# Optimization experiments

Hardware: AMD Instinct MI355X
Metric: run time of the kernel (lower is better)

## Reference

```python
import jax, jax.numpy as jnp
import numpy as np

N_NODES = 100000
N_EDGES = 3200000
IN_DIM = 128
OUT_DIM = 128
BN_EPS = 1e-5
FILL_VALUE = 1.0  # improved_gcn=False -> self-loop weight 1.0 (2.0 if improved)


def setup_inputs() -> dict:
    key = jax.random.key(0)
    k1, k2, k3, k4 = jax.random.split(key, 4)
    node_features = jax.random.normal(k1, (N_NODES, IN_DIM), dtype=jnp.float32)
    edge_index = jax.random.randint(k2, (2, N_EDGES), 0, N_NODES, dtype=jnp.int64)
    edge_weight = jax.random.uniform(k3, (N_EDGES,), dtype=jnp.float32)
    # Glorot init like PyG GCNConv
    W = jax.random.normal(k4, (IN_DIM, OUT_DIM), dtype=jnp.float32) * np.sqrt(2.0 / (IN_DIM + OUT_DIM))
    b = jnp.zeros((OUT_DIM,), dtype=jnp.float32)
    gamma = jnp.ones((OUT_DIM,), dtype=jnp.float32)
    beta = jnp.zeros((OUT_DIM,), dtype=jnp.float32)
    return {"node_features": node_features, "edge_index": edge_index,
            "edge_weight": edge_weight, "W": W, "b": b, "gamma": gamma, "beta": beta}


def reference(node_features, edge_index, edge_weight, W, b, gamma, beta):
    N = node_features.shape[0]
    dt = node_features.dtype
    # --- gcn_norm: add self loops, symmetric normalization ---
    loop = jnp.arange(N, dtype=edge_index.dtype)
    row = jnp.concatenate([edge_index[0], loop])  # source
    col = jnp.concatenate([edge_index[1], loop])  # target (aggregation dim)
    w = jnp.concatenate([edge_weight.astype(dt), jnp.full((N,), FILL_VALUE, dtype=dt)])
    deg = jax.ops.segment_sum(w, col, num_segments=N)
    dinv = jnp.where(deg > 0, jax.lax.rsqrt(deg), 0.0).astype(dt)
    norm = dinv[row] * w * dinv[col]  # [E+N]
    # --- linear transform then message passing (scatter-add into targets) ---
    x = node_features @ W  # [N, out_dim]
    msg = x[row] * norm[:, None]  # [E+N, out_dim] gather
    out = jax.ops.segment_sum(msg, col, num_segments=N) + b
    # --- relu ---
    h = jax.nn.relu(out)
    # --- BatchNorm1d (training-mode batch statistics, biased variance) ---
    mean = jnp.mean(h, axis=0)
    var = jnp.mean(jnp.square(h - mean), axis=0)
    h = (h - mean) * jax.lax.rsqrt(var + BN_EPS) * gamma + beta
    # dropout is identity in eval / deterministic reference
    return h
```

## Files before the change

### kernel.cpp

```cpp
#include <hip/hip_runtime.h>
#include <hip/hip_bf16.h>


#define BKT_BITS 7
#define BKT_SZ 128
#define MAX_BKT 1024
#define CHUNK 8192

typedef __attribute__((ext_vector_type(8))) short bf16x8;
typedef __attribute__((ext_vector_type(4))) float f32x4;

__device__ __forceinline__ unsigned bf16rn(float f) {
    unsigned x = __float_as_uint(f);
    return (x + 0x7fffu + ((x >> 16) & 1u)) >> 16;
}
__device__ __forceinline__ float bflo(unsigned u) { return __uint_as_float(u << 16); }
__device__ __forceinline__ float bfhi(unsigned u) { return __uint_as_float(u & 0xffff0000u); }

__global__ __launch_bounds__(256) void k_bhist2(const int* __restrict__ col,
        int* __restrict__ blkoff, int E, int nb, int nbc) {
    __shared__ int h[MAX_BKT];
    for (int i = threadIdx.x; i < nb; i += 256) h[i] = 0;
    __syncthreads();
    int base = blockIdx.x * CHUNK, lim = min(base + CHUNK, E);
    for (int e = base + threadIdx.x; e < lim; e += 256)
        atomicAdd(&h[col[e] >> BKT_BITS], 1);
    __syncthreads();
    for (int i = threadIdx.x; i < nb; i += 256)
        blkoff[(size_t)i * nbc + blockIdx.x] = h[i];
}

__global__ void k_bscan2a(int* __restrict__ blkoff, int* __restrict__ btot,
                          int nb, int nbc) {
    int b = blockIdx.x * 256 + threadIdx.x;
    if (b >= nb) return;
    int* p = blkoff + (size_t)b * nbc;
    int run = 0;
#pragma unroll 4
    for (int i = 0; i < nbc; ++i) { int c = p[i]; p[i] = run; run += c; }
    btot[b] = run;
}

__global__ __launch_bounds__(1024) void k_bscan2b(const int* __restrict__ btot,
        int* __restrict__ bbase, int* __restrict__ ptr, float* __restrict__ sums,
        int nb, int N, int E) {
    __shared__ int ls[1024];
    int t = threadIdx.x;
    int v = (t < nb) ? btot[t] : 0;
    ls[t] = v;
    __syncthreads();
    for (int off = 1; off < 1024; off <<= 1) {
        int u = (t >= off) ? ls[t - off] : 0;
        __syncthreads();
        ls[t] += u;
        __syncthreads();
    }
    if (t < nb) bbase[t] = ls[t] - v;
    if (t == nb - 1) bbase[nb] = ls[t];
    if (t == 0) ptr[N] = E;
    if (t < 512) sums[t] = 0.0f;
}

__global__ __launch_bounds__(256) void k_passA3(
        const int* __restrict__ row, const int* __restrict__ col,
        const float* __restrict__ w, const int* __restrict__ blkoff,
        const int* __restrict__ bbase, unsigned* __restrict__ tmp,
        int E, int nb, int nbc) {
    __shared__ int cur[MAX_BKT];
    for (int i = threadIdx.x; i < nb; i += 256)
        cur[i] = bbase[i] + blkoff[(size_t)i * nbc + blockIdx.x];
    __syncthreads();
    int base = blockIdx.x * CHUNK, lim = min(base + CHUNK, E);
    for (int e = base + threadIdx.x; e < lim; e += 256) {
        int c = col[e];
        int q8 = (int)(w[e] * 256.0f + 0.5f);
        if (q8 > 255) q8 = 255;
        unsigned rec = ((unsigned)row[e] << 15) | ((unsigned)(c & 127) << 8) | (unsigned)q8;
        int pos = atomicAdd(&cur[c >> BKT_BITS], 1);
        tmp[pos] = rec;
    }
}

__global__ __launch_bounds__(256) void k_passB2(
        const unsigned* __restrict__ tmp, const int* __restrict__ bbase,
        unsigned* __restrict__ packed, int* __restrict__ ptr,
        float* __restrict__ dinv, int N) {
    __shared__ int hcnt[BKT_SZ];
    __shared__ int wsumi[BKT_SZ];
    __shared__ int cur[BKT_SZ];
    __shared__ float dcl[BKT_SZ];
    int b = blockIdx.x;
    int t = threadIdx.x;
    if (t < BKT_SZ) { hcnt[t] = 0; wsumi[t] = 0; }
    __syncthreads();
    int beg = bbase[b], end = bbase[b + 1];
    for (int k = beg + t; k < end; k += 256) {
        unsigned p = tmp[k];
        int li = (p >> 8) & 127;
        atomicAdd(&hcnt[li], 1);
        atomicAdd(&wsumi[li], (int)(p & 255u));
    }
    __syncthreads();
    if (t < BKT_SZ) cur[t] = hcnt[t];
    __syncthreads();
    for (int off = 1; off < BKT_SZ; off <<= 1) {
        int v = (t < BKT_SZ && t >= off) ? cur[t - off] : 0;
        __syncthreads();
        if (t < BKT_SZ) cur[t] += v;
        __syncthreads();
    }
    if (t < BKT_SZ) {
        int p = beg + cur[t] - hcnt[t];
        cur[t] = p;
        float d = 1.0f + (float)wsumi[t] * (1.0f / 256.0f);
        float dc = rsqrtf(d);
        dcl[t] = dc;
        int n = (b << BKT_BITS) + t;
        if (n < N) { ptr[n] = p; dinv[n] = dc; }
    }
    __syncthreads();
    for (int k = beg + t; k < end; k += 256) {
        unsigned p = tmp[k];
        int li = (p >> 8) & 127;
        int pos = atomicAdd(&cur[li], 1);
        float fq = (float)(p & 255u) * dcl[li] * 128.0f;
        int q = (int)(fq + 0.5f);
        if (q > 32767) q = 32767;
        packed[pos] = ((p >> 15) << 15) | (unsigned)q;
    }
}

__global__ void k_conv2(const float* __restrict__ nf, const float* __restrict__ dinv,
                        uint4* __restrict__ tab, int N) {
    size_t i = (size_t)blockIdx.x * 256 + threadIdx.x;
    if (i >= (size_t)N * 16) return;
    int n = (int)(i >> 4);
    float dv = dinv[n];
    const float4* src = (const float4*)nf + 2 * i;
    float4 a = src[0], b = src[1];
    uint4 r;
    r.x = bf16rn(a.x * dv) | (bf16rn(a.y * dv) << 16);
    r.y = bf16rn(a.z * dv) | (bf16rn(a.w * dv) << 16);
    r.z = bf16rn(b.x * dv) | (bf16rn(b.y * dv) << 16);
    r.w = bf16rn(b.z * dv) | (bf16rn(b.w * dv) << 16);
    tab[i] = r;
}

__global__ void k_convW(const float* __restrict__ W, unsigned* __restrict__ WT) {
    int i = blockIdx.x * 256 + threadIdx.x;
    if (i >= 128 * 64) return;
    int j = i >> 6, w = i & 63;
    float a = W[(size_t)(2 * w) * 128 + j];
    float b = W[(size_t)(2 * w + 1) * 128 + j];
    WT[i] = bf16rn(a) | (bf16rn(b) << 16);
}

#define EDGE_FMA(aX, nX, tX)                                     \
    aX[0] += nX * bflo(tX.x); aX[1] += nX * bfhi(tX.x);          \
    aX[2] += nX * bflo(tX.y); aX[3] += nX * bfhi(tX.y);          \
    aX[4] += nX * bflo(tX.z); aX[5] += nX * bfhi(tX.z);          \
    aX[6] += nX * bflo(tX.w); aX[7] += nX * bfhi(tX.w);

__global__ __launch_bounds__(256) void k_gatherw5(
        const unsigned* __restrict__ packed, const int* __restrict__ ptr,
        const float* __restrict__ dinv, const unsigned* __restrict__ tab,
        unsigned* __restrict__ aggb, int N) {
    int wid = (int)(((size_t)blockIdx.x * 256 + threadIdx.x) >> 6);
    int lane = threadIdx.x & 63;
    if (wid >= N) return;
    int beg = ptr[wid], end = ptr[wid + 1];
    float dc = dinv[wid];
    int q = lane >> 4;
    int fl = lane & 15;
    const float sc = 1.0f / 32768.0f;
    float a0[8] = {}, a1[8] = {}, a2[8] = {}, a3[8] = {};
    int k = beg;
    for (; k + 16 <= end; k += 16) {
        unsigned p0 = packed[k + q];
        unsigned p1 = packed[k + 4 + q];
        unsigned p2 = packed[k + 8 + q];
        unsigned p3 = packed[k + 12 + q];
        uint4 t0 = *(const uint4*)(tab + (size_t)(p0 >> 15) * 64 + fl * 4);
        uint4 t1 = *(const uint4*)(tab + (size_t)(p1 >> 15) * 64 + fl * 4);
        uint4 t2 = *(const uint4*)(tab + (size_t)(p2 >> 15) * 64 + fl * 4);
        uint4 t3 = *(const uint4*)(tab + (size_t)(p3 >> 15) * 64 + fl * 4);
        float n0 = (float)(p0 & 0x7FFFu) * sc;
        float n1 = (float)(p1 & 0x7FFFu) * sc;
        float n2 = (float)(p2 & 0x7FFFu) * sc;
        float n3 = (float)(p3 & 0x7FFFu) * sc;
        EDGE_FMA(a0, n0, t0)
        EDGE_FMA(a1, n1, t1)
        EDGE_FMA(a2, n2, t2)
        EDGE_FMA(a3, n3, t3)
    }
    if (k + 8 <= end) {
        unsigned p0 = packed[k + q];
        unsigned p1 = packed[k + 4 + q];
        uint4 t0 = *(const uint4*)(tab + (size_t)(p0 >> 15) * 64 + fl * 4);
        uint4 t1 = *(const uint4*)(tab + (size_t)(p1 >> 15) * 64 + fl * 4);
        float n0 = (float)(p0 & 0x7FFFu) * sc;
        float n1 = (float)(p1 & 0x7FFFu) * sc;
        EDGE_FMA(a0, n0, t0)
        EDGE_FMA(a1, n1, t1)
        k += 8;
    }
    for (; k < end; k += 4) {
        int i0 = k + q;
        if (i0 < end) {
            unsigned p0 = packed[i0];
            uint4 t0 = *(const uint4*)(tab + (size_t)(p0 >> 15) * 64 + fl * 4);
            float n0 = (float)(p0 & 0x7FFFu) * sc;
            EDGE_FMA(a0, n0, t0)
        }
    }
#pragma unroll
    for (int j = 0; j < 8; ++j) {
        float s = (a0[j] + a1[j]) + (a2[j] + a3[j]);
        s += __shfl_xor(s, 16);
        s += __shfl_xor(s, 32);
        a0[j] = s;
    }
    if (q == 0) {
        uint4 t = *(const uint4*)(tab + (size_t)wid * 64 + fl * 4);
        EDGE_FMA(a0, dc, t)
        uint4 r;
        r.x = bf16rn(a0[0]) | (bf16rn(a0[1]) << 16);
        r.y = bf16rn(a0[2]) | (bf16rn(a0[3]) << 16);
        r.z = bf16rn(a0[4]) | (bf16rn(a0[5]) << 16);
        r.w = bf16rn(a0[6]) | (bf16rn(a0[7]) << 16);
        *(uint4*)(aggb + (size_t)wid * 64 + fl * 4) = r;
    }
}

__global__ __launch_bounds__(256) void k_gatherwF(
        const unsigned* __restrict__ packed, const int* __restrict__ ptr,
        const float* __restrict__ dinv, const unsigned* __restrict__ tab,
        float* __restrict__ out, int N) {
    int wid = (int)(((size_t)blockIdx.x * 256 + threadIdx.x) >> 6);
    int lane = threadIdx.x & 63;
    if (wid >= N) return;
    int beg = ptr[wid], end = ptr[wid + 1];
    float dc = dinv[wid];
    int q = lane >> 4;
    int fl = lane & 15;
    const float sc = 1.0f / 32768.0f;
    float a0[8] = {}, a1[8] = {};
    int k = beg;
    for (; k + 8 <= end; k += 8) {
        unsigned p0 = packed[k + q];
        unsigned p1 = packed[k + 4 + q];
        uint4 t0 = *(const uint4*)(tab + (size_t)(p0 >> 15) * 64 + fl * 4);
        uint4 t1 = *(const uint4*)(tab + (size_t)(p1 >> 15) * 64 + fl * 4);
        float n0 = (float)(p0 & 0x7FFFu) * sc;
        float n1 = (float)(p1 & 0x7FFFu) * sc;
        EDGE_FMA(a0, n0, t0)
        EDGE_FMA(a1, n1, t1)
    }
    for (; k < end; k += 4) {
        int i0 = k + q;
        if (i0 < end) {
            unsigned p0 = packed[i0];
            uint4 t0 = *(const uint4*)(tab + (size_t)(p0 >> 15) * 64 + fl * 4);
            float n0 = (float)(p0 & 0x7FFFu) * sc;
            EDGE_FMA(a0, n0, t0)
        }
    }
#pragma unroll
    for (int j = 0; j < 8; ++j) {
        float s = a0[j] + a1[j];
        s += __shfl_xor(s, 16);
        s += __shfl_xor(s, 32);
        a0[j] = s;
    }
    if (q == 0) {
        uint4 t = *(const uint4*)(tab + (size_t)wid * 64 + fl * 4);
        EDGE_FMA(a0, dc, t)
        float4* dst = (float4*)(out + (size_t)wid * 128 + fl * 8);
        dst[0] = make_float4(a0[0], a0[1], a0[2], a0[3]);
        dst[1] = make_float4(a0[4], a0[5], a0[6], a0[7]);
    }
}

__global__ __launch_bounds__(256) void k_gemm3b(
        unsigned* aggb, const unsigned* __restrict__ WT,
        const float* __restrict__ bias, float* __restrict__ sums, int N) {
    __shared__ unsigned A_l[128][68];
    __shared__ unsigned W_l[128][68];
    __shared__ float bs[256];
    int tid = threadIdx.x;
    int r0 = blockIdx.x * 128;
    bs[tid] = 0.0f;
    {
        int j = tid >> 1, h = tid & 1;
        const uint4* src = (const uint4*)(WT + j * 64 + h * 32);
#pragma unroll
        for (int i = 0; i < 8; ++i)
            *(uint4*)&W_l[j][h * 32 + i * 4] = src[i];
    }
    {
        int j = tid >> 1, h = tid & 1;
        int gr = r0 + j;
        if (gr < N) {
            const uint4* src = (const uint4*)(aggb + (size_t)gr * 64 + h * 32);
#pragma unroll
            for (int i = 0; i < 8; ++i)
                *(uint4*)&A_l[j][h * 32 + i * 4] = src[i];
        } else {
            uint4 z = {0, 0, 0, 0};
#pragma unroll
            for (int i = 0; i < 8; ++i)
                *(uint4*)&A_l[j][h * 32 + i * 4] = z;
        }
    }
    __syncthreads();

    int wv = tid >> 6, l = tid & 63;
    int lr = l & 15, lk = l >> 4;
    f32x4 acc[2][8] = {};
#pragma unroll
    for (int ks = 0; ks < 4; ++ks) {
        bf16x8 a0 = *(bf16x8*)&A_l[wv * 32 + lr][ks * 16 + lk * 4];
        bf16x8 a1 = *(bf16x8*)&A_l[wv * 32 + 16 + lr][ks * 16 + lk * 4];
#pragma unroll
        for (int nt = 0; nt < 8; ++nt) {
            bf16x8 b = *(bf16x8*)&W_l[nt * 16 + lr][ks * 16 + lk * 4];
            acc[0][nt] = __builtin_amdgcn_mfma_f32_16x16x32_bf16(a0, b, acc[0][nt], 0, 0, 0);
            acc[1][nt] = __builtin_amdgcn_mfma_f32_16x16x32_bf16(a1, b, acc[1][nt], 0, 0, 0);
        }
    }

    unsigned short* ab = (unsigned short*)aggb;
#pragma unroll
    for (int nt = 0; nt < 8; ++nt) {
        int colc = nt * 16 + lr;
        float bc = bias[colc];
        float s = 0.0f, sq = 0.0f;
#pragma unroll
        for (int ms = 0; ms < 2; ++ms) {
#pragma unroll
            for (int p = 0; p < 4; ++p) {
                int rrow = r0 + wv * 32 + ms * 16 + lk * 4 + p;
                float v = fmaxf(acc[ms][nt][p] + bc, 0.0f);
                if (rrow < N) {
                    ab[(size_t)rrow * 128 + colc] = (unsigned short)bf16rn(v);
                    s += v;
                    sq += v * v;
                }
            }
        }
        s += __shfl_xor(s, 16);  s += __shfl_xor(s, 32);
        sq += __shfl_xor(sq, 16); sq += __shfl_xor(sq, 32);
        if (l < 16) {
            atomicAdd(&bs[colc], s);
            atomicAdd(&bs[128 + colc], sq);
        }
    }
    __syncthreads();
    if (tid < 128) {
        atomicAdd(&sums[tid], bs[tid]);
        atomicAdd(&sums[128 + tid], bs[128 + tid]);
    }
}

__global__ void k_bnfin(float* __restrict__ sums, const float* __restrict__ gamma,
                        const float* __restrict__ beta, int N) {
    int j = threadIdx.x;
    float inv_n = 1.0f / (float)N;
    float mean = sums[j] * inv_n;
    float var = sums[128 + j] * inv_n - mean * mean;
    float sc = rsqrtf(var + 1e-5f) * gamma[j];
    sums[256 + j] = sc;
    sums[384 + j] = beta[j] - mean * sc;
}

__global__ void k_bnapplyB(const unsigned* __restrict__ aggb,
                           const float* __restrict__ sums,
                           float* __restrict__ out, size_t n16) {
    size_t i = (size_t)blockIdx.x * 256 + threadIdx.x;
    if (i >= n16) return;
    int g = (int)(i & 15);
    uint4 v = ((const uint4*)aggb)[i];
    float4 sc0 = *(const float4*)(sums + 256 + g * 8);
    float4 sc1 = *(const float4*)(sums + 256 + g * 8 + 4);
    float4 sh0 = *(const float4*)(sums + 384 + g * 8);
    float4 sh1 = *(const float4*)(sums + 384 + g * 8 + 4);
    float4 o0, o1;
    o0.x = bflo(v.x) * sc0.x + sh0.x;
    o0.y = bfhi(v.x) * sc0.y + sh0.y;
    o0.z = bflo(v.y) * sc0.z + sh0.z;
    o0.w = bfhi(v.y) * sc0.w + sh0.w;
    o1.x = bflo(v.z) * sc1.x + sh1.x;
    o1.y = bfhi(v.z) * sc1.y + sh1.y;
    o1.z = bflo(v.w) * sc1.z + sh1.z;
    o1.w = bfhi(v.w) * sc1.w + sh1.w;
    ((float4*)out)[2 * i] = o0;
    ((float4*)out)[2 * i + 1] = o1;
}

__global__ void k_bnapply(float* __restrict__ h, const float* __restrict__ sums, size_t n4) {
    size_t i = (size_t)blockIdx.x * 256 + threadIdx.x;
    if (i >= n4) return;
    int j4 = (int)(i & 31);
    float4 v = ((float4*)h)[i];
    float4 sc = ((const float4*)(sums + 256))[j4];
    float4 sh = ((const float4*)(sums + 384))[j4];
    v.x = v.x * sc.x + sh.x;
    v.y = v.y * sc.y + sh.y;
    v.z = v.z * sc.z + sh.z;
    v.w = v.w * sc.w + sh.w;
    ((float4*)h)[i] = v;
}

__global__ void k_init0(int* __restrict__ bcnt, float* __restrict__ sums, int nb) {
    int i = blockIdx.x * 256 + threadIdx.x;
    if (i < nb) bcnt[i] = 0;
    if (blockIdx.x == 0 && threadIdx.x < 512) sums[threadIdx.x] = 0.0f;
}
__global__ __launch_bounds__(256) void k_bhist(const int* __restrict__ col,
                                               int* __restrict__ bcnt, int E, int nb) {
    __shared__ int h[MAX_BKT];
    for (int i = threadIdx.x; i < nb; i += 256) h[i] = 0;
    __syncthreads();
    int base = blockIdx.x * CHUNK, lim = min(base + CHUNK, E);
    for (int e = base + threadIdx.x; e < lim; e += 256)
        atomicAdd(&h[col[e] >> BKT_BITS], 1);
    __syncthreads();
    for (int i = threadIdx.x; i < nb; i += 256) {
        int c = h[i];
        if (c) atomicAdd(&bcnt[i], c);
    }
}
__global__ __launch_bounds__(1024) void k_bscan(const int* __restrict__ bcnt,
        int* __restrict__ bbase, int* __restrict__ bcur,
        int* __restrict__ ptr, int nb, int N, int E) {
    __shared__ int ls[1024];
    int t = threadIdx.x;
    int v = (t < nb) ? bcnt[t] : 0;
    ls[t] = v;
    __syncthreads();
    for (int off = 1; off < 1024; off <<= 1) {
        int u = (t >= off) ? ls[t - off] : 0;
        __syncthreads();
        ls[t] += u;
        __syncthreads();
    }
    if (t < nb) {
        int ex = ls[t] - v;
        bbase[t] = ex;
        bcur[t] = ex;
    }
    if (t == nb - 1) bbase[nb] = ls[t];
    if (t == 0) ptr[N] = E;
}
__global__ __launch_bounds__(256) void k_passA2(
        const int* __restrict__ row, const int* __restrict__ col,
        const float* __restrict__ w, int* __restrict__ bcur,
        unsigned* __restrict__ tmp, int E, int nb) {
    __shared__ int h[MAX_BKT];
    for (int i = threadIdx.x; i < nb; i += 256) h[i] = 0;
    __syncthreads();
    int base = blockIdx.x * CHUNK, lim = min(base + CHUNK, E);
    for (int e = base + threadIdx.x; e < lim; e += 256)
        atomicAdd(&h[col[e] >> BKT_BITS], 1);
    __syncthreads();
    for (int i = threadIdx.x; i < nb; i += 256) {
        int c = h[i];
        if (c) h[i] = atomicAdd(&bcur[i], c);
    }
    __syncthreads();
    for (int e = base + threadIdx.x; e < lim; e += 256) {
        int c = col[e];
        int q8 = (int)(w[e] * 256.0f + 0.5f);
        if (q8 > 255) q8 = 255;
        unsigned rec = ((unsigned)row[e] << 15) | ((unsigned)(c & 127) << 8) | (unsigned)q8;
        int pos = atomicAdd(&h[c >> BKT_BITS], 1);
        tmp[pos] = rec;
    }
}

__global__ void k_init(int* __restrict__ cnt, float* __restrict__ sums, int N) {
    int i = blockIdx.x * 256 + threadIdx.x;
    if (i < N) cnt[i] = 0;
    if (blockIdx.x == 0 && threadIdx.x < 512) sums[threadIdx.x] = 0.0f;
}
__global__ void k_count(const int* __restrict__ col, int* __restrict__ cnt, int E) {
    int e = blockIdx.x * 256 + threadIdx.x;
    if (e < E) atomicAdd(&cnt[col[e]], 1);
}
__global__ __launch_bounds__(256) void kS1(const int* __restrict__ cnt,
                                           int* __restrict__ ptr,
                                           int* __restrict__ bsum, int N) {
    __shared__ int ls[256];
    int t = threadIdx.x, i = blockIdx.x * 256 + t;
    int v = (i < N) ? cnt[i] : 0;
    ls[t] = v;
    __syncthreads();
    for (int off = 1; off < 256; off <<= 1) {
        int u = (t >= off) ? ls[t - off] : 0;
        __syncthreads();
        ls[t] += u;
        __syncthreads();
    }
    if (i < N) ptr[i] = ls[t] - v;
    if (t == 255) bsum[blockIdx.x] = ls[255];
}
__global__ __launch_bounds__(512) void kS2(int* __restrict__ bsum,
                                           int* __restrict__ ptr, int NB, int N) {
    __shared__ int ls[512];
    int t = threadIdx.x;
    int chunk = (NB + 511) / 512;
    int b = t * chunk, e = min(b + chunk, NB);
    int s = 0;
    for (int i = b; i < e; ++i) s += bsum[i];
    ls[t] = s;
    __syncthreads();
    for (int off = 1; off < 512; off <<= 1) {
        int u = (t >= off) ? ls[t - off] : 0;
        __syncthreads();
        ls[t] += u;
        __syncthreads();
    }
    int run = ls[t] - s;
    for (int i = b; i < e; ++i) { int c = bsum[i]; bsum[i] = run; run += c; }
    if (t == 511) ptr[N] = ls[511];
}
__global__ void kS3(int* __restrict__ ptr, int* __restrict__ cnt,
                    const int* __restrict__ bsum, int N) {
    int i = blockIdx.x * 256 + threadIdx.x;
    if (i >= N) return;
    int p = ptr[i] + bsum[blockIdx.x];
    ptr[i] = p;
    cnt[i] = p;
}
__global__ void k_fill(const int* __restrict__ row, const int* __restrict__ col,
                       const float* __restrict__ w, int* __restrict__ cursor,
                       int2* __restrict__ packed, int E) {
    int e = blockIdx.x * 256 + threadIdx.x;
    if (e < E) {
        int pos = atomicAdd(&cursor[col[e]], 1);
        packed[pos] = make_int2(row[e], __float_as_int(w[e]));
    }
}
__global__ __launch_bounds__(256) void k_degw(const int2* __restrict__ packed,
                                              const int* __restrict__ ptr,
                                              float* __restrict__ dinv, int N) {
    int wid = (int)(((size_t)blockIdx.x * 256 + threadIdx.x) >> 6);
    int lane = threadIdx.x & 63;
    if (wid >= N) return;
    int beg = ptr[wid], end = ptr[wid + 1];
    float s = 0.0f;
    for (int k = beg + lane; k < end; k += 64) s += __int_as_float(packed[k].y);
#pragma unroll
    for (int off = 32; off; off >>= 1) s += __shfl_xor(s, off);
    if (lane == 0) {
        float d = 1.0f + s;
        dinv[wid] = d > 0.0f ? rsqrtf(d) : 0.0f;
    }
}
__global__ __launch_bounds__(256) void k_gather(
        const int2* __restrict__ packed, const int* __restrict__ ptr,
        const float* __restrict__ dinv, const float* __restrict__ nf,
        float* __restrict__ out, int N) {
    int wid = (int)(((size_t)blockIdx.x * 256 + threadIdx.x) >> 6);
    int lane = threadIdx.x & 63;
    if (wid >= N) return;
    int c = wid;
    int beg = ptr[c], end = ptr[c + 1];
    float dc = dinv[c];
    int half = lane >> 5;
    int fl = lane & 31;
    float4 acc = {0.f, 0.f, 0.f, 0.f};
    for (int k = beg; k < end; k += 2) {
        int idx = k + half;
        bool v = idx < end;
        int2 p = packed[v ? idx : beg];
        float nrm = v ? dc * __int_as_float(p.y) * dinv[p.x] : 0.0f;
        float4 x = ((const float4*)(nf + (size_t)p.x * 128))[fl];
        acc.x += nrm * x.x; acc.y += nrm * x.y;
        acc.z += nrm * x.z; acc.w += nrm * x.w;
    }
    acc.x += __shfl_xor(acc.x, 32);
    acc.y += __shfl_xor(acc.y, 32);
    acc.z += __shfl_xor(acc.z, 32);
    acc.w += __shfl_xor(acc.w, 32);
    if (half == 0) {
        float s2 = dc * dc;
        float4 sf = ((const float4*)(nf + (size_t)c * 128))[fl];
        acc.x += s2 * sf.x; acc.y += s2 * sf.y;
        acc.z += s2 * sf.z; acc.w += s2 * sf.w;
        ((float4*)(out + (size_t)c * 128))[fl] = acc;
    }
}
__global__ void k_initA(float* __restrict__ deg, float* __restrict__ sums, int N) {
    int i = blockIdx.x * 256 + threadIdx.x;
    if (i < N) deg[i] = 1.0f;
    if (blockIdx.x == 0 && threadIdx.x < 512) sums[threadIdx.x] = 0.0f;
}
__global__ void k_deg(const int* __restrict__ col, const float* __restrict__ w,
                      float* __restrict__ deg, int E) {
    int e = blockIdx.x * 256 + threadIdx.x;
    if (e < E) atomicAdd(&deg[col[e]], w[e]);
}
__global__ void k_dinv(float* __restrict__ deg, int N) {
    int i = blockIdx.x * 256 + threadIdx.x;
    if (i < N) { float d = deg[i]; deg[i] = d > 0.0f ? rsqrtf(d) : 0.0f; }
}
__global__ void k_self(const float* __restrict__ nf, const float* __restrict__ dinv,
                       float* __restrict__ agg, int N) {
    size_t i = (size_t)blockIdx.x * 256 + threadIdx.x;
    if (i >= (size_t)N * 32) return;
    int node = (int)(i >> 5);
    float s = dinv[node]; s = s * s;
    float4 v = ((const float4*)nf)[i];
    v.x *= s; v.y *= s; v.z *= s; v.w *= s;
    ((float4*)agg)[i] = v;
}
__global__ __launch_bounds__(256) void k_scatter(
        const int* __restrict__ row, const int* __restrict__ col,
        const float* __restrict__ w, const float* __restrict__ dinv,
        const float* __restrict__ nf, float* __restrict__ agg, int E) {
    int wid = (int)(((size_t)blockIdx.x * blockDim.x + threadIdx.x) >> 6);
    int lane = threadIdx.x & 63;
    if (wid >= E) return;
    int r = row[wid], c = col[wid];
    float nrm = dinv[r] * w[wid] * dinv[c];
    float2 v = ((const float2*)(nf + (size_t)r * 128))[lane];
    float* dst = agg + (size_t)c * 128 + lane * 2;
    atomicAdd(dst, v.x * nrm);
    atomicAdd(dst + 1, v.y * nrm);
}

__global__ __launch_bounds__(256) void k_gemm2(float* __restrict__ h,
        const float* __restrict__ W, const float* __restrict__ bias,
        float* __restrict__ sums, int N) {
    __shared__ float At[2][32][132];
    __shared__ float Wt[2][32][132];
    int tid = threadIdx.x;
    int tx = tid & 15, ty = tid >> 4;
    int r0 = blockIdx.x * 128;
#define STAGE_A(buf, k0)                                                     \
    _Pragma("unroll")                                                        \
    for (int i = 0; i < 4; ++i) {                                            \
        int idx = tid + 256 * i;                                             \
        int row = idx >> 3, c4 = idx & 7;                                    \
        int gr = r0 + row; if (gr > N - 1) gr = N - 1;                       \
        float4 v = *(const float4*)&h[(size_t)gr * 128 + (k0) + c4 * 4];     \
        At[buf][c4 * 4 + 0][row] = v.x;                                      \
        At[buf][c4 * 4 + 1][row] = v.y;                                      \
        At[buf][c4 * 4 + 2][row] = v.z;                                      \
        At[buf][c4 * 4 + 3][row] = v.w;                                      \
    }
#define STAGE_W(buf, k0)                                                     \
    _Pragma("unroll")                                                        \
    for (int i = 0; i < 4; ++i) {                                            \
        int idx = tid + 256 * i;                                             \
        int kk = idx >> 5, c4 = idx & 31;                                    \
        float4 v = *(const float4*)&W[(size_t)((k0) + kk) * 128 + c4 * 4];   \
        *(float4*)&Wt[buf][kk][c4 * 4] = v;                                  \
    }
    STAGE_A(0, 0)
    STAGE_W(0, 0)
    float acc[8][8] = {};
    for (int t = 0; t < 4; ++t) {
        __syncthreads();
        if (t < 3) {
            int nb = (t + 1) & 1;
            STAGE_A(nb, (t + 1) * 32)
            STAGE_W(nb, (t + 1) * 32)
        }
        int kb = t & 1;
#pragma unroll
        for (int k = 0; k < 32; ++k) {
            float a[8], w[8];
            *(float4*)&a[0] = *(float4*)&At[kb][k][ty * 8];
            *(float4*)&a[4] = *(float4*)&At[kb][k][ty * 8 + 4];
            *(float4*)&w[0] = *(float4*)&Wt[kb][k][tx * 8];
            *(float4*)&w[4] = *(float4*)&Wt[kb][k][tx * 8 + 4];
#pragma unroll
            for (int r = 0; r < 8; ++r)
#pragma unroll
                for (int cc = 0; cc < 8; ++cc)
                    acc[r][cc] += a[r] * w[cc];
        }
    }
    float bv[8];
    *(float4*)&bv[0] = *(const float4*)&bias[tx * 8];
    *(float4*)&bv[4] = *(const float4*)&bias[tx * 8 + 4];
    float s[8] = {}, sq[8] = {};
#pragma unroll
    for (int r = 0; r < 8; ++r) {
        int gr = r0 + ty * 8 + r;
        if (gr < N) {
            float o[8];
#pragma unroll
            for (int cc = 0; cc < 8; ++cc) {
                o[cc] = fmaxf(acc[r][cc] + bv[cc], 0.0f);
                s[cc] += o[cc];
                sq[cc] += o[cc] * o[cc];
            }
            float4* dst = (float4*)&h[(size_t)gr * 128 + tx * 8];
            dst[0] = make_float4(o[0], o[1], o[2], o[3]);
            dst[1] = make_float4(o[4], o[5], o[6], o[7]);
        }
    }
    float* ls = &At[0][0][0];
    __syncthreads();
#pragma unroll
    for (int cc = 0; cc < 8; ++cc) {
        ls[ty * 128 + tx * 8 + cc] = s[cc];
        ls[2048 + ty * 128 + tx * 8 + cc] = sq[cc];
    }
    __syncthreads();
    if (tid < 128) {
        float ssum = 0.f, sqsum = 0.f;
#pragma unroll
        for (int u = 0; u < 16; ++u) {
            ssum += ls[u * 128 + tid];
            sqsum += ls[2048 + u * 128 + tid];
        }
        atomicAdd(&sums[tid], ssum);
        atomicAdd(&sums[128 + tid], sqsum);
    }
#undef STAGE_A
#undef STAGE_W
}

extern "C" void kernel_launch(void* const* d_in, const int* in_sizes, int n_in,
                              void* d_out, int out_size, void* d_ws, size_t ws_size,
                              hipStream_t stream) {
    const float* nf    = (const float*)d_in[0];
    const int*   ei    = (const int*)d_in[1];
    const float* ew    = (const float*)d_in[2];
    const float* W     = (const float*)d_in[3];
    const float* bias  = (const float*)d_in[4];
    const float* gamma = (const float*)d_in[5];
    const float* beta  = (const float*)d_in[6];
    float* out = (float*)d_out;

    const int N = in_sizes[0] / 128;
    const int E = in_sizes[2];
    const int* row = ei;
    const int* col = ei + E;

    int nb_n  = (N + 255) / 256;
    int nb_e  = (E + 255) / 256;
    int nb_w  = (int)(((size_t)N + 3) / 4);
    int nb_v4 = (int)(((size_t)N * 32 + 255) / 256);
    int nbk   = (N + BKT_SZ - 1) >> BKT_BITS;
    int nb_c  = (E + CHUNK - 1) / CHUNK;
    int nconv = (int)(((size_t)N * 16 + 255) / 256);
    size_t n16 = (size_t)N * 16;
    size_t tt_words = (size_t)64 * N > (size_t)E ? (size_t)64 * N : (size_t)E;

    float* dinv = (float*)d_ws;
    int*   ptr  = (int*)d_ws + N;
    float* sums = (float*)d_ws + 2 * N + 1;
    int*   bbase1 = (int*)d_ws + 2 * N + 513;
    int*   btot   = bbase1 + nbk + 1;
    int*   blkoff = btot + nbk;
    size_t wt_off = ((size_t)(2 * N + 514 + 2 * nbk) + (size_t)nbk * nb_c + 3) & ~(size_t)3;
    unsigned* wtb = (unsigned*)((int*)d_ws + wt_off);
    size_t pk_off = (wt_off + 8192 + 3) & ~(size_t)3;
    unsigned* p1_packed = (unsigned*)((int*)d_ws + pk_off);
    size_t tt_off = (pk_off + (size_t)E + 3) & ~(size_t)3;
    unsigned* p1_tmp = (unsigned*)((int*)d_ws + tt_off);
    unsigned* p1_tab = (unsigned*)((int*)d_ws + tt_off);
    size_t ab_off = (tt_off + tt_words + 3) & ~(size_t)3;
    unsigned* aggb = (unsigned*)((int*)d_ws + ab_off);
    size_t need_p1 = (ab_off + (size_t)64 * N) * 4;

    float* dinv2 = (float*)d_ws;
    int*   ptr2  = (int*)d_ws + N;
    int*   cnt3  = (int*)d_ws + 2 * N + 1;
    float* sums2 = (float*)d_ws + 3 * N + 1;
    int*   bsum2 = (int*)d_ws + 3 * N + 513;
    int*   bbase2 = (int*)d_ws + 3 * N + 1025;
    int*   bcur2  = bbase2 + nbk + 1;
    size_t pk2 = ((size_t)(3 * N + 1026 + 2 * nbk) + 3) & ~(size_t)3;
    unsigned* packed2 = (unsigned*)((int*)d_ws + pk2);
    size_t tt2 = (pk2 + (size_t)E + 3) & ~(size_t)3;
    unsigned* tmp2 = (unsigned*)((int*)d_ws + tt2);
    unsigned* tab2 = (unsigned*)((int*)d_ws + tt2);
    size_t need_full2 = (tt2 + tt_words) * 4;

    int2*  packed3 = (int2*)((int*)d_ws + pk2);
    size_t need_csr3 = (pk2 + (size_t)2 * E) * 4;

    if (nbk <= MAX_BKT && ws_size >= need_p1) {
        k_convW<<<32, 256, 0, stream>>>(W, wtb);
        k_bhist2<<<nb_c, 256, 0, stream>>>(col, blkoff, E, nbk, nb_c);
        k_bscan2a<<<(nbk + 255) / 256, 256, 0, stream>>>(blkoff, btot, nbk, nb_c);
        k_bscan2b<<<1, 1024, 0, stream>>>(btot, bbase1, ptr, sums, nbk, N, E);
        k_passA3<<<nb_c, 256, 0, stream>>>(row, col, ew, blkoff, bbase1, p1_tmp, E, nbk, nb_c);
        k_passB2<<<nbk, 256, 0, stream>>>(p1_tmp, bbase1, p1_packed, ptr, dinv, N);
        k_conv2<<<nconv, 256, 0, stream>>>(nf, dinv, (uint4*)p1_tab, N);
        k_gatherw5<<<nb_w, 256, 0, stream>>>(p1_packed, ptr, dinv, p1_tab, aggb, N);
        k_gemm3b<<<(N + 127) / 128, 256, 0, stream>>>(aggb, wtb, bias, sums, N);
        k_bnfin<<<1, 128, 0, stream>>>(sums, gamma, beta, N);
        k_bnapplyB<<<(int)((n16 + 255) / 256), 256, 0, stream>>>(aggb, sums, out, n16);
        return;
    }

    if (nbk <= MAX_BKT && ws_size >= need_full2) {
        k_init0<<<(max(nbk, 512) + 255) / 256, 256, 0, stream>>>(bcur2, sums2, nbk);
        k_bhist<<<nb_c, 256, 0, stream>>>(col, bcur2, E, nbk);
        k_bscan<<<1, 1024, 0, stream>>>(bcur2, bbase2, bcur2, ptr2, nbk, N, E);
        k_passA2<<<nb_c, 256, 0, stream>>>(row, col, ew, bcur2, tmp2, E, nbk);
        k_passB2<<<nbk, 256, 0, stream>>>(tmp2, bbase2, packed2, ptr2, dinv2, N);
        k_conv2<<<nconv, 256, 0, stream>>>(nf, dinv2, (uint4*)tab2, N);
        k_gatherwF<<<nb_w, 256, 0, stream>>>(packed2, ptr2, dinv2, tab2, out, N);
        k_gemm2<<<(N + 127) / 128, 256, 0, stream>>>(out, W, bias, sums2, N);
        k_bnfin<<<1, 128, 0, stream>>>(sums2, gamma, beta, N);
        k_bnapply<<<nb_v4, 256, 0, stream>>>(out, sums2, (size_t)N * 32);
        return;
    }

    if (ws_size >= need_csr3) {
        k_init<<<nb_n, 256, 0, stream>>>(cnt3, sums2, N);
        k_count<<<nb_e, 256, 0, stream>>>(col, cnt3, E);
        kS1<<<nb_n, 256, 0, stream>>>(cnt3, ptr2, bsum2, N);
        kS2<<<1, 512, 0, stream>>>(bsum2, ptr2, nb_n, N);
        kS3<<<nb_n, 256, 0, stream>>>(ptr2, cnt3, bsum2, N);
        k_fill<<<nb_e, 256, 0, stream>>>(row, col, ew, cnt3, packed3, E);
        k_degw<<<nb_w, 256, 0, stream>>>(packed3, ptr2, dinv2, N);
        k_gather<<<nb_w, 256, 0, stream>>>(packed3, ptr2, dinv2, nf, out, N);
        k_gemm2<<<(N + 127) / 128, 256, 0, stream>>>(out, W, bias, sums2, N);
        k_bnfin<<<1, 128, 0, stream>>>(sums2, gamma, beta, N);
        k_bnapply<<<nb_v4, 256, 0, stream>>>(out, sums2, (size_t)N * 32);
        return;
    }

    {
        float* deg = (float*)d_ws;
        float* sm  = (float*)d_ws + N;
        k_initA<<<nb_n, 256, 0, stream>>>(deg, sm, N);
        k_deg<<<nb_e, 256, 0, stream>>>(col, ew, deg, E);
        k_dinv<<<nb_n, 256, 0, stream>>>(deg, N);
        k_self<<<nb_v4, 256, 0, stream>>>(nf, deg, out, N);
        k_scatter<<<(E + 3) / 4, 256, 0, stream>>>(row, col, ew, deg, nf, out, E);
        k_gemm2<<<(N + 127) / 128, 256, 0, stream>>>(out, W, bias, sm, N);
        k_bnfin<<<1, 128, 0, stream>>>(sm, gamma, beta, N);
        k_bnapply<<<nb_v4, 256, 0, stream>>>(out, sm, (size_t)N * 32);
    }
}
```

Measured before the change: 317.5 us.

## Map one node per quarter-wave in gather, fold W conversion and BN finalize into neighbors

The gather kernel now assigns one node to each 16-lane quarter-wave instead of one node per full wave. This removes the cross-lane shuffle reduction and the idle lanes on low-degree nodes, at the cost of more per-lane sequential edge loads and load imbalance across quarter-waves. Edge norms are stored as truncated bf16 bits rather than 15-bit fixed point, so decoding is a shift instead of a convert and multiply, with a small change in precision. The W-to-bf16 conversion moves into block 0 of the histogram kernel, and the BN finalize step is recomputed in shared memory inside the apply kernel, removing two launches.

```diff
diff --git a/kernel.cpp b/kernel.cpp
--- a/kernel.cpp
+++ b/kernel.cpp
@@ -18,7 +18,8 @@
 __device__ __forceinline__ float bfhi(unsigned u) { return __uint_as_float(u & 0xffff0000u); }
 
 __global__ __launch_bounds__(256) void k_bhist2(const int* __restrict__ col,
-        int* __restrict__ blkoff, int E, int nb, int nbc) {
+        int* __restrict__ blkoff, const float* __restrict__ Wm,
+        unsigned* __restrict__ WT, int E, int nb, int nbc) {
     __shared__ int h[MAX_BKT];
     for (int i = threadIdx.x; i < nb; i += 256) h[i] = 0;
     __syncthreads();
@@ -28,6 +29,14 @@
     __syncthreads();
     for (int i = threadIdx.x; i < nb; i += 256)
         blkoff[(size_t)i * nbc + blockIdx.x] = h[i];
+    if (blockIdx.x == 0) {
+        for (int i = threadIdx.x; i < 128 * 64; i += 256) {
+            int j = i >> 6, w = i & 63;
+            float a = Wm[(size_t)(2 * w) * 128 + j];
+            float b = Wm[(size_t)(2 * w + 1) * 128 + j];
+            WT[i] = bf16rn(a) | (bf16rn(b) << 16);
+        }
+    }
 }
 
 __global__ void k_bscan2a(int* __restrict__ blkoff, int* __restrict__ btot,
@@ -123,10 +132,9 @@
         unsigned p = tmp[k];
         int li = (p >> 8) & 127;
         int pos = atomicAdd(&cur[li], 1);
-        float fq = (float)(p & 255u) * dcl[li] * 128.0f;
-        int q = (int)(fq + 0.5f);
-        if (q > 32767) q = 32767;
-        packed[pos] = ((p >> 15) << 15) | (unsigned)q;
+        float fw = (float)(p & 255u) * (1.0f / 256.0f) * dcl[li];
+        unsigned wb = bf16rn(fw) & 0x7FFFu;
+        packed[pos] = ((p >> 15) << 15) | wb;
     }
 }
 
@@ -146,90 +154,61 @@
     tab[i] = r;
 }
 
-__global__ void k_convW(const float* __restrict__ W, unsigned* __restrict__ WT) {
-    int i = blockIdx.x * 256 + threadIdx.x;
-    if (i >= 128 * 64) return;
-    int j = i >> 6, w = i & 63;
-    float a = W[(size_t)(2 * w) * 128 + j];
-    float b = W[(size_t)(2 * w + 1) * 128 + j];
-    WT[i] = bf16rn(a) | (bf16rn(b) << 16);
-}
-
 #define EDGE_FMA(aX, nX, tX)                                     \
     aX[0] += nX * bflo(tX.x); aX[1] += nX * bfhi(tX.x);          \
     aX[2] += nX * bflo(tX.y); aX[3] += nX * bfhi(tX.y);          \
     aX[4] += nX * bflo(tX.z); aX[5] += nX * bfhi(tX.z);          \
     aX[6] += nX * bflo(tX.w); aX[7] += nX * bfhi(tX.w);
 
-__global__ __launch_bounds__(256) void k_gatherw5(
+__global__ __launch_bounds__(256) void k_gatherq(
         const unsigned* __restrict__ packed, const int* __restrict__ ptr,
         const float* __restrict__ dinv, const unsigned* __restrict__ tab,
         unsigned* __restrict__ aggb, int N) {
+    int lane = threadIdx.x & 63;
+    int q = lane >> 4, fl = lane & 15;
     int wid = (int)(((size_t)blockIdx.x * 256 + threadIdx.x) >> 6);
-    int lane = threadIdx.x & 63;
-    if (wid >= N) return;
-    int beg = ptr[wid], end = ptr[wid + 1];
-    float dc = dinv[wid];
-    int q = lane >> 4;
-    int fl = lane & 15;
-    const float sc = 1.0f / 32768.0f;
+    int node = wid * 4 + q;
+    if (node >= N) return;
+    int beg = ptr[node], end = ptr[node + 1];
+    float dc = dinv[node];
     float a0[8] = {}, a1[8] = {}, a2[8] = {}, a3[8] = {};
     int k = beg;
-    for (; k + 16 <= end; k += 16) {
-        unsigned p0 = packed[k + q];
-        unsigned p1 = packed[k + 4 + q];
-        unsigned p2 = packed[k + 8 + q];
-        unsigned p3 = packed[k + 12 + q];
+    for (; k + 4 <= end; k += 4) {
+        unsigned p0 = packed[k];
+        unsigned p1 = packed[k + 1];
+        unsigned p2 = packed[k + 2];
+        unsigned p3 = packed[k + 3];
         uint4 t0 = *(const uint4*)(tab + (size_t)(p0 >> 15) * 64 + fl * 4);
         uint4 t1 = *(const uint4*)(tab + (size_t)(p1 >> 15) * 64 + fl * 4);
         uint4 t2 = *(const uint4*)(tab + (size_t)(p2 >> 15) * 64 + fl * 4);
         uint4 t3 = *(const uint4*)(tab + (size_t)(p3 >> 15) * 64 + fl * 4);
-        float n0 = (float)(p0 & 0x7FFFu) * sc;
-        float n1 = (float)(p1 & 0x7FFFu) * sc;
-        float n2 = (float)(p2 & 0x7FFFu) * sc;
-        float n3 = (float)(p3 & 0x7FFFu) * sc;
+        float n0 = bflo(p0 & 0x7FFFu);
+        float n1 = bflo(p1 & 0x7FFFu);
+        float n2 = bflo(p2 & 0x7FFFu);
+        float n3 = bflo(p3 & 0x7FFFu);
         EDGE_FMA(a0, n0, t0)
         EDGE_FMA(a1, n1, t1)
         EDGE_FMA(a2, n2, t2)
         EDGE_FMA(a3, n3, t3)
     }
-    if (k + 8 <= end) {
-        unsigned p0 = packed[k + q];
-        unsigned p1 = packed[k + 4 + q];
-        uint4 t0 = *(const uint4*)(tab + (size_t)(p0 >> 15) * 64 + fl * 4);
-        uint4 t1 = *(const uint4*)(tab + (size_t)(p1 >> 15) * 64 + fl * 4);
-        float n0 = (float)(p0 & 0x7FFFu) * sc;
-        float n1 = (float)(p1 & 0x7FFFu) * sc;
-        EDGE_FMA(a0, n0, t0)
-        EDGE_FMA(a1, n1, t1)
-        k += 8;
-    }
-    for (; k < end; k += 4) {
-        int i0 = k + q;
-        if (i0 < end) {
-            unsigned p0 = packed[i0];
-            uint4 t0 = *(const uint4*)(tab + (size_t)(p0 >> 15) * 64 + fl * 4);
-            float n0 = (float)(p0 & 0x7FFFu) * sc;
-            EDGE_FMA(a0, n0, t0)
-        }
-    }
-#pragma unroll
-    for (int j = 0; j < 8; ++j) {
-        float s = (a0[j] + a1[j]) + (a2[j] + a3[j]);
-        s += __shfl_xor(s, 16);
-        s += __shfl_xor(s, 32);
-        a0[j] = s;
-    }
-    if (q == 0) {
-        uint4 t = *(const uint4*)(tab + (size_t)wid * 64 + fl * 4);
+    for (; k < end; ++k) {
+        unsigned p = packed[k];
+        uint4 t = *(const uint4*)(tab + (size_t)(p >> 15) * 64 + fl * 4);
+        float n = bflo(p & 0x7FFFu);
+        EDGE_FMA(a0, n, t)
+    }
+    {
+        uint4 t = *(const uint4*)(tab + (size_t)node * 64 + fl * 4);
         EDGE_FMA(a0, dc, t)
-        uint4 r;
-        r.x = bf16rn(a0[0]) | (bf16rn(a0[1]) << 16);
-        r.y = bf16rn(a0[2]) | (bf16rn(a0[3]) << 16);
-        r.z = bf16rn(a0[4]) | (bf16rn(a0[5]) << 16);
-        r.w = bf16rn(a0[6]) | (bf16rn(a0[7]) << 16);
-        *(uint4*)(aggb + (size_t)wid * 64 + fl * 4) = r;
-    }
+    }
+#pragma unroll
+    for (int j = 0; j < 8; ++j) a0[j] = (a0[j] + a1[j]) + (a2[j] + a3[j]);
+    uint4 r;
+    r.x = bf16rn(a0[0]) | (bf16rn(a0[1]) << 16);
+    r.y = bf16rn(a0[2]) | (bf16rn(a0[3]) << 16);
+    r.z = bf16rn(a0[4]) | (bf16rn(a0[5]) << 16);
+    r.w = bf16rn(a0[6]) | (bf16rn(a0[7]) << 16);
+    *(uint4*)(aggb + (size_t)node * 64 + fl * 4) = r;
 }
 
 __global__ __launch_bounds__(256) void k_gatherwF(
@@ -243,7 +222,6 @@
     float dc = dinv[wid];
     int q = lane >> 4;
     int fl = lane & 15;
-    const float sc = 1.0f / 32768.0f;
     float a0[8] = {}, a1[8] = {};
     int k = beg;
     for (; k + 8 <= end; k += 8) {
@@ -251,8 +229,8 @@
         unsigned p1 = packed[k + 4 + q];
         uint4 t0 = *(const uint4*)(tab + (size_t)(p0 >> 15) * 64 + fl * 4);
         uint4 t1 = *(const uint4*)(tab + (size_t)(p1 >> 15) * 64 + fl * 4);
-        float n0 = (float)(p0 & 0x7FFFu) * sc;
-        float n1 = (float)(p1 & 0x7FFFu) * sc;
+        float n0 = bflo(p0 & 0x7FFFu);
+        float n1 = bflo(p1 & 0x7FFFu);
         EDGE_FMA(a0, n0, t0)
         EDGE_FMA(a1, n1, t1)
     }
@@ -261,7 +239,7 @@
         if (i0 < end) {
             unsigned p0 = packed[i0];
             uint4 t0 = *(const uint4*)(tab + (size_t)(p0 >> 15) * 64 + fl * 4);
-            float n0 = (float)(p0 & 0x7FFFu) * sc;
+            float n0 = bflo(p0 & 0x7FFFu);
             EDGE_FMA(a0, n0, t0)
         }
     }
@@ -362,28 +340,29 @@
     }
 }
 
-__global__ void k_bnfin(float* __restrict__ sums, const float* __restrict__ gamma,
-                        const float* __restrict__ beta, int N) {
-    int j = threadIdx.x;
-    float inv_n = 1.0f / (float)N;
-    float mean = sums[j] * inv_n;
-    float var = sums[128 + j] * inv_n - mean * mean;
-    float sc = rsqrtf(var + 1e-5f) * gamma[j];
-    sums[256 + j] = sc;
-    sums[384 + j] = beta[j] - mean * sc;
-}
-
-__global__ void k_bnapplyB(const unsigned* __restrict__ aggb,
-                           const float* __restrict__ sums,
-                           float* __restrict__ out, size_t n16) {
+__global__ __launch_bounds__(256) void k_bnapplyB2(
+        const unsigned* __restrict__ aggb, const float* __restrict__ sums,
+        const float* __restrict__ gamma, const float* __restrict__ beta,
+        float* __restrict__ out, size_t n16, int N) {
+    __shared__ float sc[128], sh[128];
+    int t = threadIdx.x;
+    if (t < 128) {
+        float inv_n = 1.0f / (float)N;
+        float mean = sums[t] * inv_n;
+        float var = sums[128 + t] * inv_n - mean * mean;
+        float s = rsqrtf(var + 1e-5f) * gamma[t];
+        sc[t] = s;
+        sh[t] = beta[t] - mean * s;
+    }
+    __syncthreads();
     size_t i = (size_t)blockIdx.x * 256 + threadIdx.x;
     if (i >= n16) return;
     int g = (int)(i & 15);
     uint4 v = ((const uint4*)aggb)[i];
-    float4 sc0 = *(const float4*)(sums + 256 + g * 8);
-    float4 sc1 = *(const float4*)(sums + 256 + g * 8 + 4);
-    float4 sh0 = *(const float4*)(sums + 384 + g * 8);
-    float4 sh1 = *(const float4*)(sums + 384 + g * 8 + 4);
+    float4 sc0 = *(float4*)&sc[g * 8];
+    float4 sc1 = *(float4*)&sc[g * 8 + 4];
+    float4 sh0 = *(float4*)&sh[g * 8];
+    float4 sh1 = *(float4*)&sh[g * 8 + 4];
     float4 o0, o1;
     o0.x = bflo(v.x) * sc0.x + sh0.x;
     o0.y = bfhi(v.x) * sc0.y + sh0.y;
@@ -395,6 +374,17 @@
     o1.w = bfhi(v.w) * sc1.w + sh1.w;
     ((float4*)out)[2 * i] = o0;
     ((float4*)out)[2 * i + 1] = o1;
+}
+
+__global__ void k_bnfin(float* __restrict__ sums, const float* __restrict__ gamma,
+                        const float* __restrict__ beta, int N) {
+    int j = threadIdx.x;
+    float inv_n = 1.0f / (float)N;
+    float mean = sums[j] * inv_n;
+    float var = sums[128 + j] * inv_n - mean * mean;
+    float sc = rsqrtf(var + 1e-5f) * gamma[j];
+    sums[256 + j] = sc;
+    sums[384 + j] = beta[j] - mean * sc;
 }
 
 __global__ void k_bnapply(float* __restrict__ h, const float* __restrict__ sums, size_t n4) {
@@ -745,6 +735,7 @@
     int nb_n  = (N + 255) / 256;
     int nb_e  = (E + 255) / 256;
     int nb_w  = (int)(((size_t)N + 3) / 4);
+    int nb_q  = (N + 15) / 16;
     int nb_v4 = (int)(((size_t)N * 32 + 255) / 256);
     int nbk   = (N + BKT_SZ - 1) >> BKT_BITS;
     int nb_c  = (E + CHUNK - 1) / CHUNK;
@@ -787,17 +778,15 @@
     size_t need_csr3 = (pk2 + (size_t)2 * E) * 4;
 
     if (nbk <= MAX_BKT && ws_size >= need_p1) {
-        k_convW<<<32, 256, 0, stream>>>(W, wtb);
-        k_bhist2<<<nb_c, 256, 0, stream>>>(col, blkoff, E, nbk, nb_c);
+        k_bhist2<<<nb_c, 256, 0, stream>>>(col, blkoff, W, wtb, E, nbk, nb_c);
         k_bscan2a<<<(nbk + 255) / 256, 256, 0, stream>>>(blkoff, btot, nbk, nb_c);
         k_bscan2b<<<1, 1024, 0, stream>>>(btot, bbase1, ptr, sums, nbk, N, E);
         k_passA3<<<nb_c, 256, 0, stream>>>(row, col, ew, blkoff, bbase1, p1_tmp, E, nbk, nb_c);
         k_passB2<<<nbk, 256, 0, stream>>>(p1_tmp, bbase1, p1_packed, ptr, dinv, N);
         k_conv2<<<nconv, 256, 0, stream>>>(nf, dinv, (uint4*)p1_tab, N);
-        k_gatherw5<<<nb_w, 256, 0, stream>>>(p1_packed, ptr, dinv, p1_tab, aggb, N);
+        k_gatherq<<<nb_q, 256, 0, stream>>>(p1_packed, ptr, dinv, p1_tab, aggb, N);
         k_gemm3b<<<(N + 127) / 128, 256, 0, stream>>>(aggb, wtb, bias, sums, N);
-        k_bnfin<<<1, 128, 0, stream>>>(sums, gamma, beta, N);
-        k_bnapplyB<<<(int)((n16 + 255) / 256), 256, 0, stream>>>(aggb, sums, out, n16);
+        k_bnapplyB2<<<(int)((n16 + 255) / 256), 256, 0, stream>>>(aggb, sums, gamma, beta, out, n16, N);
         return;
     }
 
```

After: 337.3 us. 1.06x slower.
